# Performance work log

Measured on AMD Instinct MI355X. Metric: run time of the kernel, lower is better.

Reference implementation:

```python
import jax, jax.numpy as jnp
import numpy as np

NP_CONST = 48.0  # Np in the original code


def dft_matrices(freq=48, time=512):
    # A[t, f] = exp(-2j*pi*t*f/time)/sqrt(time), split into re/im, shape [time, freq]
    t = np.arange(time)[:, None]
    f = np.arange(freq)[None, :]
    ang = -2.0 * np.pi * t * f / time
    scale = 1.0 / np.sqrt(time)
    return (np.cos(ang) * scale).astype(np.float32), (np.sin(ang) * scale).astype(np.float32)


def _mm(xr, xi, wr, wi):
    # complex matmul: (xr + i xi) @ (wr + i wi)
    return xr @ wr - xi @ wi, xr @ wi + xi @ wr


def _act(R, sigma, theta):
    # scaled soft-threshold (standard LAMP shrinkage); returns f and df/dR
    lam = theta[0] * sigma
    mag = jnp.abs(R)
    shr = jnp.maximum(mag - lam, 0.0)
    f = theta[1] * jnp.sign(R) * shr
    df = theta[1] * (mag > lam).astype(R.dtype)
    return f, df


def setup_inputs() -> dict:
    key = jax.random.key(0)
    L, B = 8, 8192
    dre, dim = dft_matrices(48, 512)
    u = jax.random.normal(key, (B, 48, 2), dtype=jnp.float32)
    # per-layer params initialized to the DFT matrices (as in LAMP_layer.__init__)
    A_re = jnp.broadcast_to(jnp.asarray(dre), (L, 512, 48)).copy()
    A_im = jnp.broadcast_to(jnp.asarray(dim), (L, 512, 48)).copy()
    theta = jnp.broadcast_to(jnp.array([1.0, 1.0, -1.0], dtype=jnp.float32), (L, 3)).copy()
    return {"u": u, "A_re": A_re, "A_im": A_im, "theta": theta,
            "DFT_re": jnp.asarray(dre), "DFT_im": jnp.asarray(dim)}


def _lamp_forward(u, A_re, A_im, theta, DFT_re, DFT_im):
    u_re, u_im = u[:, :, 0], u[:, :, 1]          # [B, 48]
    B = u_re.shape[0]
    z_re, z_im = u_re, u_im
    H_re = jnp.zeros((B, 512), dtype=u.dtype)
    H_im = jnp.zeros((B, 512), dtype=u.dtype)

    def layer(carry, params):
        z_re, z_im, H_re, H_im = carry
        Are, Aim, th = params                      # [512,48], [512,48], [3]
        # Z = z @ A.T : [B,48] x [48,512]
        Z_re, Z_im = _mm(z_re, z_im, Are.T, Aim.T)
        R_re = H_re + Z_re
        R_im = H_im + Z_im
        sigma = jnp.sqrt(jnp.sum(z_re * z_re) + jnp.sum(z_im * z_im)) / jnp.sqrt(NP_CONST)
        Hn_re, d_re = _act(R_re, sigma, th)
        Hn_im, d_im = _act(R_im, sigma, th)
        b_re = d_re.sum() / NP_CONST
        b_im = d_im.sum() / NP_CONST
        # h_hat = H_hat @ A : [B,512] x [512,48]
        h_re, h_im = _mm(Hn_re, Hn_im, Are, Aim)
        zn_re = u_re - h_re + b_re * z_re
        zn_im = u_im - h_im + b_im * z_im
        return (zn_re, zn_im, Hn_re, Hn_im), None

    (z_re, z_im, H_re, H_im), _ = jax.lax.scan(layer, (z_re, z_im, H_re, H_im),
                                               (A_re, A_im, theta))
    h_re, h_im = _mm(H_re, H_im, DFT_re, DFT_im)   # [B, 48]
    return jnp.stack((h_re, h_im), axis=2)          # [B, 48, 2]


def reference(u, A_re, A_im, theta, DFT_re, DFT_im):
    return _lamp_forward(u, A_re, A_im, theta, DFT_re, DFT_im)
```

## Files before the change

kernel.cpp:

```cpp
#include <hip/hip_runtime.h>
#include <hip/hip_bf16.h>
#include <math.h>

#define B_   8192
#define F_   48
#define T_   512
#define L_   8
#define NBLK 256
#define THR  512
#define NW   8
#define RPB  32
#define HST  520
#define ZS   52
#define LINE 32

typedef unsigned short ushort_t;
typedef unsigned int   uint_t;
typedef __attribute__((ext_vector_type(8))) short short8;
typedef __attribute__((ext_vector_type(4))) float f32x4;

#define MFMA(a,b,c) __builtin_amdgcn_mfma_f32_16x16x32_bf16(a,b,c,0,0,0)

__device__ inline ushort_t f2bf(float x) {
    __hip_bfloat16 h = __float2bfloat16(x);
    return *reinterpret_cast<ushort_t*>(&h);
}
__device__ inline short8 negbf(short8 v) {
    short8 r;
    #pragma unroll
    for (int i = 0; i < 8; ++i) r[i] = v[i] ^ (short)0x8000;
    return r;
}
__device__ inline short8 pack8(float4 a, float4 b) {
    short8 r;
    r[0]=(short)f2bf(a.x); r[1]=(short)f2bf(a.y); r[2]=(short)f2bf(a.z); r[3]=(short)f2bf(a.w);
    r[4]=(short)f2bf(b.x); r[5]=(short)f2bf(b.y); r[6]=(short)f2bf(b.z); r[7]=(short)f2bf(b.w);
    return r;
}

__device__ inline float aload(const float* p) {
    return __hip_atomic_load(p, __ATOMIC_RELAXED, __HIP_MEMORY_SCOPE_AGENT);
}
__device__ inline void astore(float* p, float v) {
    __hip_atomic_store(p, v, __ATOMIC_RELAXED, __HIP_MEMORY_SCOPE_AGENT);
}
__device__ inline void afadd(float* p, float v) {
    (void)__hip_atomic_fetch_add(p, v, __ATOMIC_RELAXED, __HIP_MEMORY_SCOPE_AGENT);
}

__device__ inline void arrive(float* vbase, uint_t* cnt8, int blk,
                              float v0, float v1, int nv) {
    afadd(vbase + (blk & 7) * LINE, v0);
    if (nv > 1) afadd(vbase + (8 + (blk & 7)) * LINE, v1);
    (void)__hip_atomic_fetch_add(&cnt8[(blk & 7) * LINE], 1u,
                                 __ATOMIC_RELEASE, __HIP_MEMORY_SCOPE_AGENT);
}

__device__ inline float2 collect(uint_t* cnt8, float* vbase, float* bcbase,
                                 uint_t target, int nv) {
    for (;;) {
        uint_t s = 0;
        #pragma unroll
        for (int i = 0; i < 8; ++i)
            s += __hip_atomic_load(&cnt8[i * LINE], __ATOMIC_RELAXED, __HIP_MEMORY_SCOPE_AGENT);
        if (s >= target) break;
        __builtin_amdgcn_s_sleep(1);
    }
    (void)__hip_atomic_load(&cnt8[0], __ATOMIC_ACQUIRE, __HIP_MEMORY_SCOPE_AGENT);
    float v0 = 0.f, v1 = 0.f;
    #pragma unroll
    for (int i = 0; i < 8; ++i) v0 += aload(vbase + i * LINE);
    if (nv > 1) {
        #pragma unroll
        for (int i = 0; i < 8; ++i) v1 += aload(vbase + (8 + i) * LINE);
    }
    #pragma unroll
    for (int j = 0; j < 8; ++j) {
        astore(bcbase + j * LINE + 1, v0);
        astore(bcbase + j * LINE + 2, v1);
    }
    #pragma unroll
    for (int j = 0; j < 8; ++j)
        __hip_atomic_store((uint_t*)(bcbase + j * LINE), 1u,
                           __ATOMIC_RELEASE, __HIP_MEMORY_SCOPE_AGENT);
    return make_float2(v0, v1);
}

__device__ inline float2 waitbc(const float* bcline) {
    while (__hip_atomic_load((const uint_t*)bcline, __ATOMIC_RELAXED,
                             __HIP_MEMORY_SCOPE_AGENT) == 0u)
        __builtin_amdgcn_s_sleep(2);
    (void)__hip_atomic_load((const uint_t*)bcline, __ATOMIC_ACQUIRE,
                            __HIP_MEMORY_SCOPE_AGENT);
    return make_float2(aload(bcline + 1), aload(bcline + 2));
}

#define SYNC_DW ((8 + 16 * 8 + 16 * 16) * LINE)

__global__ __launch_bounds__(256) void k_pre(
    const float* __restrict__ Ar, const float* __restrict__ Ai,
    const float* __restrict__ Dr, const float* __restrict__ Di,
    ushort_t* __restrict__ Afr, ushort_t* __restrict__ Afi,
    ushort_t* __restrict__ Atr, ushort_t* __restrict__ Ati,
    ushort_t* __restrict__ Dfr, ushort_t* __restrict__ Dfi,
    uint_t* __restrict__ syncbuf)
{
    const int gt = blockIdx.x * 256 + threadIdx.x;
    const int gs = gridDim.x * 256;
    for (int idx = gt; idx < SYNC_DW; idx += gs) syncbuf[idx] = 0u;
    for (int idx = gt; idx < L_ * 32768; idx += gs) {
        int j = idx & 7, rest = idx >> 3;
        int mm = rest & 15; rest >>= 4;
        int qq = rest & 3;  rest >>= 2;
        int k2 = rest & 1;  rest >>= 1;
        int tile = rest & 31;
        int l = rest >> 5;
        int t = tile * 16 + mm, k = k2 * 32 + qq * 8 + j;
        float vr = 0.f, vi = 0.f;
        if (k < 48) { int g = l * 24576 + t * 48 + k; vr = Ar[g]; vi = Ai[g]; }
        Afr[idx] = f2bf(vr); Afi[idx] = f2bf(vi);
    }
    for (int idx = gt; idx < L_ * 24576; idx += gs) {
        int j = idx & 7, rest = idx >> 3;
        int mm = rest & 15; rest >>= 4;
        int qq = rest & 3;  rest >>= 2;
        int ks = rest & 15; rest >>= 4;
        int ft = rest % 3;
        int l = rest / 3;
        int f = ft * 16 + mm, k = ks * 32 + qq * 8 + j;
        int g = l * 24576 + k * 48 + f;
        Atr[idx] = f2bf(Ar[g]); Ati[idx] = f2bf(Ai[g]);
    }
    for (int idx = gt; idx < 24576; idx += gs) {
        int j = idx & 7, rest = idx >> 3;
        int mm = rest & 15; rest >>= 4;
        int qq = rest & 3;  rest >>= 2;
        int ks = rest & 15;
        int ft = rest >> 4;
        int f = ft * 16 + mm, k = ks * 32 + qq * 8 + j;
        Dfr[idx] = f2bf(Dr[k * 48 + f]); Dfi[idx] = f2bf(Di[k * 48 + f]);
    }
}

__global__ __launch_bounds__(THR, 2) void k_lamp(
    const float* __restrict__ u,
    const ushort_t* __restrict__ Afr, const ushort_t* __restrict__ Afi,
    const ushort_t* __restrict__ Atr, const ushort_t* __restrict__ Ati,
    const ushort_t* __restrict__ Dfr, const ushort_t* __restrict__ Dfi,
    const float* __restrict__ th,
    uint_t* syncbuf,
    float* __restrict__ out)
{
    extern __shared__ char dyn[];
    float*    pR   = (float*)dyn;
    float*    pI   = pR + 8 * 3 * 16 * 17;
    float*    zreL = pI + 8 * 3 * 16 * 17;
    float*    zimL = zreL + RPB * ZS;
    float*    red  = zimL + RPB * ZS;
    ushort_t* HreL = (ushort_t*)(red + 32);
    ushort_t* HimL = HreL + RPB * HST;

    uint_t* cnt8 = syncbuf;
    float*  bcF  = (float*)(syncbuf + 8 * LINE);
    float*  vals = bcF + 16 * 8 * LINE;

    const int tid = threadIdx.x, blk = blockIdx.x;
    const int row0 = blk * RPB;
    const int wave = tid >> 6, lane = tid & 63;
    const int quad = lane >> 4, m = lane & 15;
    const int rows16 = (wave >> 2) * 16;
    const int rt = wave >> 2, kq = wave & 3;
    const float2* u2 = (const float2*)u;

    auto gsync = [&](int s, int nv) {
        if (tid == 0) {
            float2 v = (blk == 0)
                ? collect(cnt8, vals + s * 16 * LINE, bcF + s * 8 * LINE,
                          (uint_t)NBLK * (uint_t)(s + 1), nv)
                : waitbc(bcF + s * 8 * LINE + (blk & 7) * LINE);
            red[0] = v.x; red[1] = v.y;
        }
        __syncthreads();
        return make_float2(red[0], red[1]);
    };

    f32x4 hR[8], hI[8];
    #pragma unroll
    for (int ct = 0; ct < 8; ++ct) { hR[ct] = (f32x4){0,0,0,0}; hI[ct] = (f32x4){0,0,0,0}; }

    float acc = 0.f;
    #pragma unroll
    for (int k3 = 0; k3 < 3; ++k3) {
        int j = tid + k3 * THR;
        int r = j / 48, c = j - r * 48;
        float2 v = u2[(row0 + r) * 48 + c];
        zreL[r * ZS + c] = v.x; zimL[r * ZS + c] = v.y;
        acc += v.x * v.x + v.y * v.y;
    }
    #pragma unroll
    for (int s = 32; s > 0; s >>= 1) acc += __shfl_xor(acc, s, 64);
    __syncthreads();
    if (lane == 0) red[8 + wave] = acc;
    __syncthreads();
    if (tid == 0) {
        float t = 0.f;
        #pragma unroll
        for (int w = 0; w < NW; ++w) t += red[8 + w];
        arrive(vals + 0, cnt8, blk, t, 0.f, 1);
    }

    for (int l = 0; l < L_; ++l) {
        const float* zpr = zreL + (rows16 + m) * ZS;
        const float* zpi = zimL + (rows16 + m) * ZS;
        short8 zr0 = pack8(*(const float4*)(zpr + quad * 8), *(const float4*)(zpr + quad * 8 + 4));
        short8 zi0 = pack8(*(const float4*)(zpi + quad * 8), *(const float4*)(zpi + quad * 8 + 4));
        short8 zr1 = {0,0,0,0,0,0,0,0}, zi1 = {0,0,0,0,0,0,0,0};
        if (quad < 2) {
            zr1 = pack8(*(const float4*)(zpr + 32 + quad * 8), *(const float4*)(zpr + 36 + quad * 8));
            zi1 = pack8(*(const float4*)(zpi + 32 + quad * 8), *(const float4*)(zpi + 36 + quad * 8));
        }
        short8 zin0 = negbf(zi0), zin1 = negbf(zi1);

        const ushort_t* Aflr = Afr + (size_t)l * 32768;
        const ushort_t* Afli = Afi + (size_t)l * 32768;
        #pragma unroll
        for (int ct = 0; ct < 8; ++ct) {
            const int tile = (wave & 3) * 8 + ct;
            const ushort_t* rp = Aflr + (size_t)(tile * 2) * 512 + lane * 8;
            const ushort_t* ip = Afli + (size_t)(tile * 2) * 512 + lane * 8;
            short8 ar0 = *(const short8*)rp;
            short8 ar1 = *(const short8*)(rp + 512);
            short8 ai0 = *(const short8*)ip;
            short8 ai1 = *(const short8*)(ip + 512);
            hR[ct] = MFMA(zr0, ar0, hR[ct]);
            hR[ct] = MFMA(zr1, ar1, hR[ct]);
            hR[ct] = MFMA(zin0, ai0, hR[ct]);
            hR[ct] = MFMA(zin1, ai1, hR[ct]);
            hI[ct] = MFMA(zr0, ai0, hI[ct]);
            hI[ct] = MFMA(zr1, ai1, hI[ct]);
            hI[ct] = MFMA(zi0, ar0, hI[ct]);
            hI[ct] = MFMA(zi1, ar1, hI[ct]);
        }

        float2 sv = gsync(2 * l, 1);
        const float lam = th[l * 3] * sqrtf(sv.x * (1.0f / 48.0f));
        const float th1 = th[l * 3 + 1];

        float cr = 0.f, ci = 0.f;
        #pragma unroll
        for (int ct = 0; ct < 8; ++ct) {
            const int t = ((wave & 3) * 8 + ct) * 16 + m;
            #pragma unroll
            for (int reg = 0; reg < 4; ++reg) {
                const int lr = rows16 + quad * 4 + reg;
                float Rr = hR[ct][reg], Ri = hI[ct][reg];
                float mr = fabsf(Rr), mi = fabsf(Ri);
                float fr = th1 * copysignf(fmaxf(mr - lam, 0.f), Rr);
                float fi = th1 * copysignf(fmaxf(mi - lam, 0.f), Ri);
                cr += (mr > lam) ? 1.f : 0.f;
                ci += (mi > lam) ? 1.f : 0.f;
                hR[ct][reg] = fr; hI[ct][reg] = fi;
                HreL[lr * HST + t] = f2bf(fr);
                HimL[lr * HST + t] = f2bf(fi);
            }
        }

        if (l == L_ - 1) { __syncthreads(); break; }

        #pragma unroll
        for (int s = 32; s > 0; s >>= 1) { cr += __shfl_xor(cr, s, 64); ci += __shfl_xor(ci, s, 64); }
        __syncthreads();
        if (lane == 0) { red[8 + wave] = cr; red[16 + wave] = ci; }
        __syncthreads();
        if (tid == 0) {
            float tr = 0.f, tii = 0.f;
            #pragma unroll
            for (int w = 0; w < NW; ++w) { tr += red[8 + w]; tii += red[16 + w]; }
            arrive(vals + (2 * l + 1) * 16 * LINE, cnt8, blk, tr, tii, 2);
        }

        const ushort_t* Atlr = Atr + (size_t)l * 24576;
        const ushort_t* Atli = Ati + (size_t)l * 24576;
        f32x4 aR[3], aI[3];
        #pragma unroll
        for (int q = 0; q < 3; ++q) { aR[q] = (f32x4){0,0,0,0}; aI[q] = (f32x4){0,0,0,0}; }
        #pragma unroll
        for (int ks = 0; ks < 4; ++ks) {
            const int ksa = kq * 4 + ks;
            const int k0 = ksa * 32 + quad * 8;
            short8 hr = *(const short8*)&HreL[(rt * 16 + m) * HST + k0];
            short8 hi = *(const short8*)&HimL[(rt * 16 + m) * HST + k0];
            short8 hin = negbf(hi);
            #pragma unroll
            for (int ft = 0; ft < 3; ++ft) {
                short8 br = *(const short8*)(Atlr + (size_t)((ft * 16 + ksa) * 64 + lane) * 8);
                short8 bi = *(const short8*)(Atli + (size_t)((ft * 16 + ksa) * 64 + lane) * 8);
                aR[ft] = MFMA(hr, br, aR[ft]);
                aR[ft] = MFMA(hin, bi, aR[ft]);
                aI[ft] = MFMA(hr, bi, aI[ft]);
                aI[ft] = MFMA(hi, br, aI[ft]);
            }
        }
        #pragma unroll
        for (int ft = 0; ft < 3; ++ft) {
            #pragma unroll
            for (int reg = 0; reg < 4; ++reg) {
                pR[((wave * 3 + ft) * 16 + quad * 4 + reg) * 17 + m] = aR[ft][reg];
                pI[((wave * 3 + ft) * 16 + quad * 4 + reg) * 17 + m] = aI[ft][reg];
            }
        }

        float2 bv = gsync(2 * l + 1, 2);
        const float bre = th1 * bv.x * (1.0f / 48.0f);
        const float bim = th1 * bv.y * (1.0f / 48.0f);

        float nrm = 0.f;
        #pragma unroll
        for (int k3 = 0; k3 < 3; ++k3) {
            int j = tid + k3 * THR;
            int r = j / 48, f = j - r * 48;
            int rt2 = r >> 4, lr = r & 15, ft = f >> 4, c = f & 15;
            float hRv = 0.f, hIv = 0.f;
            #pragma unroll
            for (int q = 0; q < 4; ++q) {
                hRv += pR[(((rt2 * 4 + q) * 3 + ft) * 16 + lr) * 17 + c];
                hIv += pI[(((rt2 * 4 + q) * 3 + ft) * 16 + lr) * 17 + c];
            }
            float2 uv = u2[(row0 + r) * 48 + f];
            float zr = zreL[r * ZS + f], zi = zimL[r * ZS + f];
            float znr = uv.x - hRv + bre * zr;
            float zni = uv.y - hIv + bim * zi;
            zreL[r * ZS + f] = znr; zimL[r * ZS + f] = zni;
            nrm += znr * znr + zni * zni;
        }
        #pragma unroll
        for (int s = 32; s > 0; s >>= 1) nrm += __shfl_xor(nrm, s, 64);
        __syncthreads();
        if (lane == 0) red[8 + wave] = nrm;
        __syncthreads();
        if (tid == 0) {
            float t = 0.f;
            #pragma unroll
            for (int w = 0; w < NW; ++w) t += red[8 + w];
            arrive(vals + (2 * l + 2) * 16 * LINE, cnt8, blk, t, 0.f, 1);
        }
    }

    f32x4 fR[3], fI[3];
    #pragma unroll
    for (int q = 0; q < 3; ++q) { fR[q] = (f32x4){0,0,0,0}; fI[q] = (f32x4){0,0,0,0}; }
    #pragma unroll
    for (int ks = 0; ks < 4; ++ks) {
        const int ksa = kq * 4 + ks;
        const int k0 = ksa * 32 + quad * 8;
        short8 hr = *(const short8*)&HreL[(rt * 16 + m) * HST + k0];
        short8 hi = *(const short8*)&HimL[(rt * 16 + m) * HST + k0];
        short8 hin = negbf(hi);
        #pragma unroll
        for (int ft = 0; ft < 3; ++ft) {
            short8 br = *(const short8*)(Dfr + (size_t)((ft * 16 + ksa) * 64 + lane) * 8);
            short8 bi = *(const short8*)(Dfi + (size_t)((ft * 16 + ksa) * 64 + lane) * 8);
            fR[ft] = MFMA(hr, br, fR[ft]);
            fR[ft] = MFMA(hin, bi, fR[ft]);
            fI[ft] = MFMA(hr, bi, fI[ft]);
            fI[ft] = MFMA(hi, br, fI[ft]);
        }
    }
    #pragma unroll
    for (int ft = 0; ft < 3; ++ft) {
        #pragma unroll
        for (int reg = 0; reg < 4; ++reg) {
            pR[((wave * 3 + ft) * 16 + quad * 4 + reg) * 17 + m] = fR[ft][reg];
            pI[((wave * 3 + ft) * 16 + quad * 4 + reg) * 17 + m] = fI[ft][reg];
        }
    }
    __syncthreads();
    float2* out2 = (float2*)out;
    #pragma unroll
    for (int k3 = 0; k3 < 3; ++k3) {
        int j = tid + k3 * THR;
        int r = j / 48, f = j - r * 48;
        int rt2 = r >> 4, lr = r & 15, ft = f >> 4, c = f & 15;
        float hRv = 0.f, hIv = 0.f;
        #pragma unroll
        for (int q = 0; q < 4; ++q) {
            hRv += pR[(((rt2 * 4 + q) * 3 + ft) * 16 + lr) * 17 + c];
            hIv += pI[(((rt2 * 4 + q) * 3 + ft) * 16 + lr) * 17 + c];
        }
        out2[(row0 + r) * 48 + f] = make_float2(hRv, hIv);
    }
}

extern "C" void kernel_launch(void* const* d_in, const int* in_sizes, int n_in,
                              void* d_out, int out_size, void* d_ws, size_t ws_size,
                              hipStream_t stream) {
    (void)in_sizes; (void)n_in; (void)out_size; (void)ws_size;
    const float* u  = (const float*)d_in[0];
    const float* Ar = (const float*)d_in[1];
    const float* Ai = (const float*)d_in[2];
    const float* th = (const float*)d_in[3];
    const float* Dr = (const float*)d_in[4];
    const float* Di = (const float*)d_in[5];
    float* out = (float*)d_out;

    char* p = (char*)d_ws;
    auto alloc = [&](size_t bytes) -> char* {
        char* r = p;
        p += (bytes + 255) & ~(size_t)255;
        return r;
    };
    uint_t*   syncbuf = (uint_t*)alloc(SYNC_DW * 4);
    ushort_t* Afr = (ushort_t*)alloc((size_t)L_ * 32768 * 2);
    ushort_t* Afi = (ushort_t*)alloc((size_t)L_ * 32768 * 2);
    ushort_t* Atr = (ushort_t*)alloc((size_t)L_ * 24576 * 2);
    ushort_t* Ati = (ushort_t*)alloc((size_t)L_ * 24576 * 2);
    ushort_t* Dfr = (ushort_t*)alloc((size_t)24576 * 2);
    ushort_t* Dfi = (ushort_t*)alloc((size_t)24576 * 2);

    k_pre<<<1024, 256, 0, stream>>>(Ar, Ai, Dr, Di, Afr, Afi, Atr, Ati, Dfr, Dfi, syncbuf);

    const uint_t lds_bytes = 132224;
    hipFuncSetAttribute((const void*)k_lamp,
                        hipFuncAttributeMaxDynamicSharedMemorySize, (int)lds_bytes);
    void* args[] = { (void*)&u, (void*)&Afr, (void*)&Afi, (void*)&Atr, (void*)&Ati,
                     (void*)&Dfr, (void*)&Dfi, (void*)&th,
                     (void*)&syncbuf, (void*)&out };
    hipLaunchCooperativeKernel((void*)k_lamp, dim3(NBLK), dim3(THR), args,
                               lds_bytes, stream);
}
```

Measured before the change: 290.2 us.

## Merge per-layer grid syncs via algebraic norm expansion and decentralized event flags

Replaces the block-0 collect/broadcast barrier with per-block event lines that every block polls and reduces itself. It also removes one of the two grid-wide syncs per layer: the next layer's sigma is derived algebraically from partial sums (|a|^2, a·z, |z|^2) combined with the not-yet-known b coefficients, so the derivative sums and the norm terms travel in a single exchange. This halves the number of grid barriers and drops the serialized hop through block 0. In exchange each block polls 256 flag lines and reduces 8 values per layer, and the expanded-norm formula can lose some floating-point accuracy through cancellation.

```diff
diff --git a/kernel.cpp b/kernel.cpp
--- a/kernel.cpp
+++ b/kernel.cpp
@@ -13,6 +13,9 @@
 #define HST  520
 #define ZS   52
 #define LINE 32
+#define EVT_DW (NBLK * LINE)
+#define NEVT 8
+#define SYNC_DW (NEVT * EVT_DW)
 
 typedef unsigned short ushort_t;
 typedef unsigned int   uint_t;
@@ -44,58 +47,42 @@
 __device__ inline void astore(float* p, float v) {
     __hip_atomic_store(p, v, __ATOMIC_RELAXED, __HIP_MEMORY_SCOPE_AGENT);
 }
-__device__ inline void afadd(float* p, float v) {
-    (void)__hip_atomic_fetch_add(p, v, __ATOMIC_RELAXED, __HIP_MEMORY_SCOPE_AGENT);
-}
-
-__device__ inline void arrive(float* vbase, uint_t* cnt8, int blk,
-                              float v0, float v1, int nv) {
-    afadd(vbase + (blk & 7) * LINE, v0);
-    if (nv > 1) afadd(vbase + (8 + (blk & 7)) * LINE, v1);
-    (void)__hip_atomic_fetch_add(&cnt8[(blk & 7) * LINE], 1u,
-                                 __ATOMIC_RELEASE, __HIP_MEMORY_SCOPE_AGENT);
-}
-
-__device__ inline float2 collect(uint_t* cnt8, float* vbase, float* bcbase,
-                                 uint_t target, int nv) {
-    for (;;) {
-        uint_t s = 0;
-        #pragma unroll
-        for (int i = 0; i < 8; ++i)
-            s += __hip_atomic_load(&cnt8[i * LINE], __ATOMIC_RELAXED, __HIP_MEMORY_SCOPE_AGENT);
-        if (s >= target) break;
-        __builtin_amdgcn_s_sleep(1);
-    }
-    (void)__hip_atomic_load(&cnt8[0], __ATOMIC_ACQUIRE, __HIP_MEMORY_SCOPE_AGENT);
-    float v0 = 0.f, v1 = 0.f;
-    #pragma unroll
-    for (int i = 0; i < 8; ++i) v0 += aload(vbase + i * LINE);
-    if (nv > 1) {
-        #pragma unroll
-        for (int i = 0; i < 8; ++i) v1 += aload(vbase + (8 + i) * LINE);
-    }
-    #pragma unroll
-    for (int j = 0; j < 8; ++j) {
-        astore(bcbase + j * LINE + 1, v0);
-        astore(bcbase + j * LINE + 2, v1);
-    }
+
+__device__ inline void publish(float* evtbase, int blk, const float* v, int nv) {
+    float* line = evtbase + (size_t)blk * LINE;
     #pragma unroll
     for (int j = 0; j < 8; ++j)
-        __hip_atomic_store((uint_t*)(bcbase + j * LINE), 1u,
-                           __ATOMIC_RELEASE, __HIP_MEMORY_SCOPE_AGENT);
-    return make_float2(v0, v1);
-}
-
-__device__ inline float2 waitbc(const float* bcline) {
-    while (__hip_atomic_load((const uint_t*)bcline, __ATOMIC_RELAXED,
-                             __HIP_MEMORY_SCOPE_AGENT) == 0u)
-        __builtin_amdgcn_s_sleep(2);
-    (void)__hip_atomic_load((const uint_t*)bcline, __ATOMIC_ACQUIRE,
-                            __HIP_MEMORY_SCOPE_AGENT);
-    return make_float2(aload(bcline + 1), aload(bcline + 2));
-}
-
-#define SYNC_DW ((8 + 16 * 8 + 16 * 16) * LINE)
+        if (j < nv) astore(line + 1 + j, v[j]);
+    __hip_atomic_store((uint_t*)line, 1u, __ATOMIC_RELEASE, __HIP_MEMORY_SCOPE_AGENT);
+}
+
+__device__ inline void evt_wait(float* evtbase, int wave, int lane, int nv, float* red) {
+    if (wave == 0) {
+        uint_t* f0 = (uint_t*)evtbase;
+        for (;;) {
+            bool ok = true;
+            #pragma unroll
+            for (int g = 0; g < NBLK / 64; ++g) {
+                uint_t fl = __hip_atomic_load(f0 + (size_t)(g * 64 + lane) * LINE,
+                                              __ATOMIC_RELAXED, __HIP_MEMORY_SCOPE_AGENT);
+                ok = ok && (fl != 0u);
+            }
+            if (__all(ok)) break;
+            __builtin_amdgcn_s_sleep(1);
+        }
+    }
+    __syncthreads();
+    if (wave < nv) {
+        float s = 0.f;
+        #pragma unroll
+        for (int g = 0; g < NBLK / 64; ++g)
+            s += aload(evtbase + (size_t)(g * 64 + lane) * LINE + 1 + wave);
+        #pragma unroll
+        for (int o = 32; o > 0; o >>= 1) s += __shfl_xor(s, o, 64);
+        if (lane == 0) red[wave] = s;
+    }
+    __syncthreads();
+}
 
 __global__ __launch_bounds__(256) void k_pre(
     const float* __restrict__ Ar, const float* __restrict__ Ai,
@@ -157,12 +144,10 @@
     float*    zreL = pI + 8 * 3 * 16 * 17;
     float*    zimL = zreL + RPB * ZS;
     float*    red  = zimL + RPB * ZS;
-    ushort_t* HreL = (ushort_t*)(red + 32);
+    ushort_t* HreL = (ushort_t*)(red + 128);
     ushort_t* HimL = HreL + RPB * HST;
 
-    uint_t* cnt8 = syncbuf;
-    float*  bcF  = (float*)(syncbuf + 8 * LINE);
-    float*  vals = bcF + 16 * 8 * LINE;
+    float* evt = (float*)syncbuf;
 
     const int tid = threadIdx.x, blk = blockIdx.x;
     const int row0 = blk * RPB;
@@ -172,18 +157,6 @@
     const int rt = wave >> 2, kq = wave & 3;
     const float2* u2 = (const float2*)u;
 
-    auto gsync = [&](int s, int nv) {
-        if (tid == 0) {
-            float2 v = (blk == 0)
-                ? collect(cnt8, vals + s * 16 * LINE, bcF + s * 8 * LINE,
-                          (uint_t)NBLK * (uint_t)(s + 1), nv)
-                : waitbc(bcF + s * 8 * LINE + (blk & 7) * LINE);
-            red[0] = v.x; red[1] = v.y;
-        }
-        __syncthreads();
-        return make_float2(red[0], red[1]);
-    };
-
     f32x4 hR[8], hI[8];
     #pragma unroll
     for (int ct = 0; ct < 8; ++ct) { hR[ct] = (f32x4){0,0,0,0}; hI[ct] = (f32x4){0,0,0,0}; }
@@ -198,18 +171,21 @@
         acc += v.x * v.x + v.y * v.y;
     }
     #pragma unroll
-    for (int s = 32; s > 0; s >>= 1) acc += __shfl_xor(acc, s, 64);
+    for (int o = 32; o > 0; o >>= 1) acc += __shfl_xor(acc, o, 64);
     __syncthreads();
-    if (lane == 0) red[8 + wave] = acc;
+    if (lane == 0) red[16 + wave] = acc;
     __syncthreads();
     if (tid == 0) {
         float t = 0.f;
         #pragma unroll
-        for (int w = 0; w < NW; ++w) t += red[8 + w];
-        arrive(vals + 0, cnt8, blk, t, 0.f, 1);
-    }
-
+        for (int w = 0; w < NW; ++w) t += red[16 + w];
+        publish(evt, blk, &t, 1);
+    }
+
+    float lam = 0.f;
     for (int l = 0; l < L_; ++l) {
+        const float th1 = th[l * 3 + 1];
+
         const float* zpr = zreL + (rows16 + m) * ZS;
         const float* zpi = zimL + (rows16 + m) * ZS;
         short8 zr0 = pack8(*(const float4*)(zpr + quad * 8), *(const float4*)(zpr + quad * 8 + 4));
@@ -242,9 +218,10 @@
             hI[ct] = MFMA(zi1, ar1, hI[ct]);
         }
 
-        float2 sv = gsync(2 * l, 1);
-        const float lam = th[l * 3] * sqrtf(sv.x * (1.0f / 48.0f));
-        const float th1 = th[l * 3 + 1];
+        if (l == 0) {
+            evt_wait(evt, wave, lane, 1, red);
+            lam = th[0] * sqrtf(red[0] * (1.0f / 48.0f));
+        }
 
         float cr = 0.f, ci = 0.f;
         #pragma unroll
@@ -266,18 +243,7 @@
         }
 
         if (l == L_ - 1) { __syncthreads(); break; }
-
-        #pragma unroll
-        for (int s = 32; s > 0; s >>= 1) { cr += __shfl_xor(cr, s, 64); ci += __shfl_xor(ci, s, 64); }
         __syncthreads();
-        if (lane == 0) { red[8 + wave] = cr; red[16 + wave] = ci; }
-        __syncthreads();
-        if (tid == 0) {
-            float tr = 0.f, tii = 0.f;
-            #pragma unroll
-            for (int w = 0; w < NW; ++w) { tr += red[8 + w]; tii += red[16 + w]; }
-            arrive(vals + (2 * l + 1) * 16 * LINE, cnt8, blk, tr, tii, 2);
-        }
 
         const ushort_t* Atlr = Atr + (size_t)l * 24576;
         const ushort_t* Atli = Ati + (size_t)l * 24576;
@@ -309,12 +275,10 @@
                 pI[((wave * 3 + ft) * 16 + quad * 4 + reg) * 17 + m] = aI[ft][reg];
             }
         }
-
-        float2 bv = gsync(2 * l + 1, 2);
-        const float bre = th1 * bv.x * (1.0f / 48.0f);
-        const float bim = th1 * bv.y * (1.0f / 48.0f);
-
-        float nrm = 0.f;
+        __syncthreads();
+
+        float aRe[3], aIm[3], zR3[3], zI3[3];
+        float S1 = 0.f, S2 = 0.f, S3 = 0.f, S4 = 0.f, S5 = 0.f, S6 = 0.f;
         #pragma unroll
         for (int k3 = 0; k3 < 3; ++k3) {
             int j = tid + k3 * THR;
@@ -328,22 +292,53 @@
             }
             float2 uv = u2[(row0 + r) * 48 + f];
             float zr = zreL[r * ZS + f], zi = zimL[r * ZS + f];
-            float znr = uv.x - hRv + bre * zr;
-            float zni = uv.y - hIv + bim * zi;
-            zreL[r * ZS + f] = znr; zimL[r * ZS + f] = zni;
-            nrm += znr * znr + zni * zni;
-        }
-        #pragma unroll
-        for (int s = 32; s > 0; s >>= 1) nrm += __shfl_xor(nrm, s, 64);
-        __syncthreads();
-        if (lane == 0) red[8 + wave] = nrm;
+            float ar = uv.x - hRv, ai = uv.y - hIv;
+            aRe[k3] = ar; aIm[k3] = ai; zR3[k3] = zr; zI3[k3] = zi;
+            S1 += ar * ar; S2 += ar * zr; S3 += zr * zr;
+            S4 += ai * ai; S5 += ai * zi; S6 += zi * zi;
+        }
+
+        float v8[8] = {cr, ci, S1, S2, S3, S4, S5, S6};
+        #pragma unroll
+        for (int j = 0; j < 8; ++j) {
+            #pragma unroll
+            for (int o = 32; o > 0; o >>= 1) v8[j] += __shfl_xor(v8[j], o, 64);
+        }
+        if (lane == 0) {
+            #pragma unroll
+            for (int j = 0; j < 8; ++j) red[16 + wave * 8 + j] = v8[j];
+        }
         __syncthreads();
         if (tid == 0) {
-            float t = 0.f;
-            #pragma unroll
-            for (int w = 0; w < NW; ++w) t += red[8 + w];
-            arrive(vals + (2 * l + 2) * 16 * LINE, cnt8, blk, t, 0.f, 1);
-        }
+            float o8[8];
+            #pragma unroll
+            for (int j = 0; j < 8; ++j) {
+                float s = 0.f;
+                #pragma unroll
+                for (int w = 0; w < NW; ++w) s += red[16 + w * 8 + j];
+                o8[j] = s;
+            }
+            publish(evt + (size_t)(l + 1) * EVT_DW, blk, o8, 8);
+        }
+
+        evt_wait(evt + (size_t)(l + 1) * EVT_DW, wave, lane, 8, red);
+        const float CR = red[0], CI = red[1];
+        const float G1 = red[2], G2 = red[3], G3 = red[4];
+        const float G4 = red[5], G5 = red[6], G6 = red[7];
+        const float bre = th1 * CR * (1.0f / 48.0f);
+        const float bim = th1 * CI * (1.0f / 48.0f);
+        const float sig2 = G1 + 2.f * bre * G2 + bre * bre * G3
+                         + G4 + 2.f * bim * G5 + bim * bim * G6;
+        lam = th[(l + 1) * 3] * sqrtf(sig2 * (1.0f / 48.0f));
+
+        #pragma unroll
+        for (int k3 = 0; k3 < 3; ++k3) {
+            int j = tid + k3 * THR;
+            int r = j / 48, f = j - r * 48;
+            zreL[r * ZS + f] = aRe[k3] + bre * zR3[k3];
+            zimL[r * ZS + f] = aIm[k3] + bim * zI3[k3];
+        }
+        __syncthreads();
     }
 
     f32x4 fR[3], fI[3];
@@ -409,7 +404,7 @@
         p += (bytes + 255) & ~(size_t)255;
         return r;
     };
-    uint_t*   syncbuf = (uint_t*)alloc(SYNC_DW * 4);
+    uint_t*   syncbuf = (uint_t*)alloc((size_t)SYNC_DW * 4);
     ushort_t* Afr = (ushort_t*)alloc((size_t)L_ * 32768 * 2);
     ushort_t* Afi = (ushort_t*)alloc((size_t)L_ * 32768 * 2);
     ushort_t* Atr = (ushort_t*)alloc((size_t)L_ * 24576 * 2);
@@ -419,7 +414,7 @@
 
     k_pre<<<1024, 256, 0, stream>>>(Ar, Ai, Dr, Di, Afr, Afi, Atr, Ati, Dfr, Dfi, syncbuf);
 
-    const uint_t lds_bytes = 132224;
+    const uint_t lds_bytes = 132608;
     hipFuncSetAttribute((const void*)k_lamp,
                         hipFuncAttributeMaxDynamicSharedMemorySize, (int)lds_bytes);
     void* args[] = { (void*)&u, (void*)&Afr, (void*)&Afi, (void*)&Atr, (void*)&Ati,
```

New measurement: 307.7 us. +6.0%, slower.
